# Optimization experiments

Hardware: AMD Instinct MI355X
Metric: run time of the kernel (lower is better)

## Reference

```python
import jax, jax.numpy as jnp
import numpy as np


def setup_inputs() -> dict:
    key = jax.random.key(0)
    k1, k2 = jax.random.split(key)
    B, T, F, C = 16, 512, 1024, 4
    # predicted soft masks in [0,1)
    masks = jax.random.uniform(k1, (B, T, F, C), dtype=jnp.float32)
    # precomputed STFT of source audio: magnitude||phase concatenated on dim 2
    src_stft = jax.random.uniform(k2, (B, T, 2 * F, C), dtype=jnp.float32)
    return {"masks": masks, "src_stft": src_stft}


def reference(masks, src_stft):
    # split: keep first half along dim 2 (magnitude part), as torch.split(..., dim=2)[0]
    F = src_stft.shape[2] // 2
    gt = jax.lax.stop_gradient(src_stft[:, :, :F, :])  # [B, T, F, C] (no_grad in original)
    C = gt.shape[-1]
    # fused argmax -> one-hot (the original's per-class Python loop)
    gt_max_idx = jnp.argmax(gt, axis=-1)               # [B, T, F], first-max like torch
    gt_onehot = jax.nn.one_hot(gt_max_idx, C, dtype=masks.dtype)  # [B, T, F, C]
    # nn.L1Loss default reduction='mean'
    loss = jnp.mean(jnp.abs(masks - gt_onehot))
    return loss
```

## Files before the change

### kernel.cpp

```cpp
#include <hip/hip_runtime.h>


#define C_PER_GROUP 4
#define F_DIM 1024
#define F_SHIFT 10
#define F_MASK 1023

__global__ __launch_bounds__(256) void recon_loss_kernel(
    const float4* __restrict__ masks,
    const float4* __restrict__ src,
    float* __restrict__ out,
    unsigned int G, float inv_n)
{
    unsigned int tid    = blockIdx.x * blockDim.x + threadIdx.x;
    unsigned int stride = gridDim.x * blockDim.x;

    float acc = 0.0f;
    for (unsigned int g = tid; g < G; g += stride) {
        unsigned int bt = g >> F_SHIFT;
        unsigned int f  = g & F_MASK;
        float4 gt = src[(bt << (F_SHIFT + 1)) | f];
        float4 m  = masks[g];

        int   idx  = 0;
        float best = gt.x;
        if (gt.y > best) { best = gt.y; idx = 1; }
        if (gt.z > best) { best = gt.z; idx = 2; }
        if (gt.w > best) { best = gt.w; idx = 3; }

        acc += fabsf(m.x - (idx == 0 ? 1.0f : 0.0f));
        acc += fabsf(m.y - (idx == 1 ? 1.0f : 0.0f));
        acc += fabsf(m.z - (idx == 2 ? 1.0f : 0.0f));
        acc += fabsf(m.w - (idx == 3 ? 1.0f : 0.0f));
    }

    #pragma unroll
    for (int off = 32; off > 0; off >>= 1)
        acc += __shfl_down(acc, off, 64);

    __shared__ float wave_sums[4];
    int lane = threadIdx.x & 63;
    int wave = threadIdx.x >> 6;
    if (lane == 0) wave_sums[wave] = acc;
    __syncthreads();

    if (threadIdx.x == 0) {
        float blk = wave_sums[0] + wave_sums[1] + wave_sums[2] + wave_sums[3];
        atomicAdd(out, blk * inv_n);
    }
}

extern "C" void kernel_launch(void* const* d_in, const int* in_sizes, int n_in,
                              void* d_out, int out_size, void* d_ws, size_t ws_size,
                              hipStream_t stream) {
    const float4* masks = (const float4*)d_in[0];
    const float4* src   = (const float4*)d_in[1];
    float* out = (float*)d_out;

    const unsigned int n_mask_elems = (unsigned int)in_sizes[0];
    const unsigned int G = n_mask_elems / C_PER_GROUP;
    const float inv_n = 1.0f / (float)n_mask_elems;

    hipMemsetAsync(d_out, 0, sizeof(float), stream);

    const int block = 256;
    const int grid  = 4096;
    recon_loss_kernel<<<grid, block, 0, stream>>>(masks, src, out, G, inv_n);
}
```

Before: 406.8 us.

## Unroll grid-stride loop with nontemporal loads and two-stage partial reduction

Rewrites the streaming loop to issue four independent mask and source loads per iteration using nontemporal loads, raising memory-level parallelism and bypassing cache retention for data read once. Replaces the memset plus per-block atomicAdd with per-block partials written to the workspace and a second single-block kernel that reduces them deterministically. The grid is halved to 2048 blocks. The extra kernel launch adds a small fixed overhead, and halving the grid relies on unrolling to keep enough loads in flight.

```diff
diff --git a/kernel.cpp b/kernel.cpp
--- a/kernel.cpp
+++ b/kernel.cpp
@@ -1,69 +1,124 @@
 #include <hip/hip_runtime.h>
 
 
-#define C_PER_GROUP 4
-#define F_DIM 1024
+typedef float f32x4 __attribute__((ext_vector_type(4)));
+
 #define F_SHIFT 10
-#define F_MASK 1023
+#define F_MASK  1023u
 
-__global__ __launch_bounds__(256) void recon_loss_kernel(
-    const float4* __restrict__ masks,
-    const float4* __restrict__ src,
-    float* __restrict__ out,
-    unsigned int G, float inv_n)
+__device__ __forceinline__ unsigned int src_idx(unsigned int g) {
+    return g + (g & ~F_MASK);
+}
+
+__device__ __forceinline__ float group_cost(f32x4 m, f32x4 t) {
+    int   idx  = 0;
+    float best = t.x;
+    if (t.y > best) { best = t.y; idx = 1; }
+    if (t.z > best) { best = t.z; idx = 2; }
+    if (t.w > best) { best = t.w; idx = 3; }
+    float s;
+    s  = fabsf(m.x - (idx == 0 ? 1.0f : 0.0f));
+    s += fabsf(m.y - (idx == 1 ? 1.0f : 0.0f));
+    s += fabsf(m.z - (idx == 2 ? 1.0f : 0.0f));
+    s += fabsf(m.w - (idx == 3 ? 1.0f : 0.0f));
+    return s;
+}
+
+__global__ __launch_bounds__(256) void recon_loss_partial(
+    const f32x4* __restrict__ masks,
+    const f32x4* __restrict__ src,
+    float* __restrict__ partials,
+    unsigned int G)
 {
-    unsigned int tid    = blockIdx.x * blockDim.x + threadIdx.x;
-    unsigned int stride = gridDim.x * blockDim.x;
+    const unsigned int nth = gridDim.x * blockDim.x;
+    const unsigned int tid = blockIdx.x * blockDim.x + threadIdx.x;
+    const unsigned int iters = G / nth;
 
     float acc = 0.0f;
-    for (unsigned int g = tid; g < G; g += stride) {
-        unsigned int bt = g >> F_SHIFT;
-        unsigned int f  = g & F_MASK;
-        float4 gt = src[(bt << (F_SHIFT + 1)) | f];
-        float4 m  = masks[g];
+    unsigned int i = 0;
 
-        int   idx  = 0;
-        float best = gt.x;
-        if (gt.y > best) { best = gt.y; idx = 1; }
-        if (gt.z > best) { best = gt.z; idx = 2; }
-        if (gt.w > best) { best = gt.w; idx = 3; }
+    for (; i + 4 <= iters; i += 4) {
+        const unsigned int g0 = tid + (i    ) * nth;
+        const unsigned int g1 = tid + (i + 1) * nth;
+        const unsigned int g2 = tid + (i + 2) * nth;
+        const unsigned int g3 = tid + (i + 3) * nth;
 
-        acc += fabsf(m.x - (idx == 0 ? 1.0f : 0.0f));
-        acc += fabsf(m.y - (idx == 1 ? 1.0f : 0.0f));
-        acc += fabsf(m.z - (idx == 2 ? 1.0f : 0.0f));
-        acc += fabsf(m.w - (idx == 3 ? 1.0f : 0.0f));
+        const f32x4 m0 = __builtin_nontemporal_load(&masks[g0]);
+        const f32x4 m1 = __builtin_nontemporal_load(&masks[g1]);
+        const f32x4 m2 = __builtin_nontemporal_load(&masks[g2]);
+        const f32x4 m3 = __builtin_nontemporal_load(&masks[g3]);
+        const f32x4 t0 = __builtin_nontemporal_load(&src[src_idx(g0)]);
+        const f32x4 t1 = __builtin_nontemporal_load(&src[src_idx(g1)]);
+        const f32x4 t2 = __builtin_nontemporal_load(&src[src_idx(g2)]);
+        const f32x4 t3 = __builtin_nontemporal_load(&src[src_idx(g3)]);
+
+        acc += group_cost(m0, t0);
+        acc += group_cost(m1, t1);
+        acc += group_cost(m2, t2);
+        acc += group_cost(m3, t3);
+    }
+    for (; i < iters; ++i) {
+        const unsigned int g = tid + i * nth;
+        acc += group_cost(__builtin_nontemporal_load(&masks[g]),
+                          __builtin_nontemporal_load(&src[src_idx(g)]));
+    }
+    for (unsigned int g = tid + iters * nth; g < G; g += nth) {
+        acc += group_cost(__builtin_nontemporal_load(&masks[g]),
+                          __builtin_nontemporal_load(&src[src_idx(g)]));
     }
 
     #pragma unroll
     for (int off = 32; off > 0; off >>= 1)
         acc += __shfl_down(acc, off, 64);
 
-    __shared__ float wave_sums[4];
-    int lane = threadIdx.x & 63;
-    int wave = threadIdx.x >> 6;
-    if (lane == 0) wave_sums[wave] = acc;
+    __shared__ float wsum[4];
+    const int lane = threadIdx.x & 63;
+    const int wave = threadIdx.x >> 6;
+    if (lane == 0) wsum[wave] = acc;
     __syncthreads();
 
-    if (threadIdx.x == 0) {
-        float blk = wave_sums[0] + wave_sums[1] + wave_sums[2] + wave_sums[3];
-        atomicAdd(out, blk * inv_n);
-    }
+    if (threadIdx.x == 0)
+        partials[blockIdx.x] = wsum[0] + wsum[1] + wsum[2] + wsum[3];
+}
+
+__global__ __launch_bounds__(256) void reduce_partials(
+    const float* __restrict__ partials,
+    float* __restrict__ out,
+    unsigned int n, float inv_n)
+{
+    float acc = 0.0f;
+    for (unsigned int i = threadIdx.x; i < n; i += 256)
+        acc += partials[i];
+
+    #pragma unroll
+    for (int off = 32; off > 0; off >>= 1)
+        acc += __shfl_down(acc, off, 64);
+
+    __shared__ float wsum[4];
+    const int lane = threadIdx.x & 63;
+    const int wave = threadIdx.x >> 6;
+    if (lane == 0) wsum[wave] = acc;
+    __syncthreads();
+
+    if (threadIdx.x == 0)
+        out[0] = (wsum[0] + wsum[1] + wsum[2] + wsum[3]) * inv_n;
 }
 
 extern "C" void kernel_launch(void* const* d_in, const int* in_sizes, int n_in,
                               void* d_out, int out_size, void* d_ws, size_t ws_size,
                               hipStream_t stream) {
-    const float4* masks = (const float4*)d_in[0];
-    const float4* src   = (const float4*)d_in[1];
-    float* out = (float*)d_out;
+    const f32x4* masks = (const f32x4*)d_in[0];
+    const f32x4* src   = (const f32x4*)d_in[1];
+    float* out      = (float*)d_out;
+    float* partials = (float*)d_ws;
 
     const unsigned int n_mask_elems = (unsigned int)in_sizes[0];
-    const unsigned int G = n_mask_elems / C_PER_GROUP;
+    const unsigned int G = n_mask_elems / 4;
     const float inv_n = 1.0f / (float)n_mask_elems;
 
-    hipMemsetAsync(d_out, 0, sizeof(float), stream);
+    const int block = 256;
+    const int grid  = 2048;
 
-    const int block = 256;
-    const int grid  = 4096;
-    recon_loss_kernel<<<grid, block, 0, stream>>>(masks, src, out, G, inv_n);
+    recon_loss_partial<<<grid, block, 0, stream>>>(masks, src, partials, G);
+    reduce_partials<<<1, block, 0, stream>>>(partials, out, (unsigned int)grid, inv_n);
 }
```

After: 383.0 us. 5.8% less time.
